# Kernel optimization log

Hardware: AMD Instinct MI355X
Metric: run time of the kernel (lower is better)

## Reference

```python
import jax, jax.numpy as jnp
import numpy as np

V, D, H, L, B, S = 8192, 128, 8, 2, 1, 128
HD = D // H
HID = int(8 * D / 3)
EPS = 1e-6


def setup_inputs() -> dict:
    key = jax.random.key(0)
    ks = jax.random.split(key, 12)
    sc = 0.02
    return {
        "idx": jax.random.randint(ks[0], (B, S), 0, V),
        "w_raw": jax.random.normal(ks[1], (D, V), jnp.float32) * sc,
        "norm1_w": jnp.ones((L, D), jnp.float32),
        "norm2_w": jnp.ones((L, D), jnp.float32),
        "wq": jax.random.normal(ks[2], (L, D, D), jnp.float32) * sc,
        "wk": jax.random.normal(ks[3], (L, D, D), jnp.float32) * sc,
        "wv": jax.random.normal(ks[4], (L, D, D), jnp.float32) * sc,
        "wo": jax.random.normal(ks[5], (L, D, D), jnp.float32) * sc,
        "w1": jax.random.normal(ks[6], (L, D, HID), jnp.float32) * sc,
        "w3": jax.random.normal(ks[7], (L, D, HID), jnp.float32) * sc,
        "w2": jax.random.normal(ks[8], (L, HID, D), jnp.float32) * sc,
        "final_norm_w": jnp.ones((D,), jnp.float32),
    }


def rmsnorm(x, w):
    return x * jax.lax.rsqrt(jnp.mean(x * x, axis=-1, keepdims=True) + EPS) * w


def rope_cos_sin(seqlen, hd):
    inv = 1.0 / (10000.0 ** (jnp.arange(0, hd, 2, dtype=jnp.float32) / hd))
    t = jnp.arange(seqlen, dtype=jnp.float32)
    f = jnp.outer(t, inv)  # (S, hd/2)
    return jnp.cos(f), jnp.sin(f)


def apply_rope(x, cos, sin):
    # x: (B,S,H,HD); interleaved complex pairs as in Llama
    x0, x1 = x[..., 0::2], x[..., 1::2]
    c = cos[None, :, None, :]
    s = sin[None, :, None, :]
    r0 = x0 * c - x1 * s
    r1 = x0 * s + x1 * c
    return jnp.stack([r0, r1], axis=-1).reshape(x.shape)


def forward(idx, w_raw, norm1_w, norm2_w, wq, wk, wv, wo, w1, w2, w3, final_norm_w):
    Wemb = jax.nn.sigmoid(w_raw)                 # (D,V)
    x = Wemb.T[idx]                              # Yoneda one-hot @ W.T == gather -> (B,S,D)
    cos, sin = rope_cos_sin(S, HD)
    causal = jnp.tril(jnp.ones((S, S), bool))[None, None]  # (1,1,S,S)
    scale = 1.0 / jnp.sqrt(jnp.float32(HD))
    for i in range(L):
        # Multi-Universe attention (heads == universes), RoPE, causal SDPA
        h = rmsnorm(x, norm1_w[i])
        q = (h @ wq[i]).reshape(B, S, H, HD)
        k = (h @ wk[i]).reshape(B, S, H, HD)
        v = (h @ wv[i]).reshape(B, S, H, HD)
        q = apply_rope(q, cos, sin)
        k = apply_rope(k, cos, sin)
        scores = jnp.einsum("bihd,bjhd->bhij", q, k) * scale
        scores = jnp.where(causal, scores, jnp.float32(-1e9))
        attn = jax.nn.softmax(scores, axis=-1)
        o = jnp.einsum("bhij,bjhd->bihd", attn, v).reshape(B, S, D) @ wo[i]
        x = x + o
        # SwiGLU FFN
        h2 = rmsnorm(x, norm2_w[i])
        x = x + (jax.nn.silu(h2 @ w1[i]) * (h2 @ w3[i])) @ w2[i]
    x_norm = rmsnorm(x, final_norm_w)
    # Godel-Heyting reachability head
    x_n = x_norm / jnp.linalg.norm(x_norm, axis=-1, keepdims=True)      # (B,S,D)
    v_n = (Wemb / jnp.linalg.norm(Wemb, axis=0, keepdims=True)).T        # (V,D)
    a = x_n[:, :, None, :]                                               # (B,S,1,D)
    b = v_n[None, None, :, :]                                            # (1,1,V,D)
    # strict Godel implication: a => b = 1 if a <= b else b
    imp = jnp.where(a <= b, jnp.float32(1.0), b)                         # (B,S,V,D)
    logits = jnp.clip(imp.mean(axis=-1), 1e-6, 1.0 - 1e-6)               # (B,S,V)
    return logits


def reference(idx, w_raw, norm1_w, norm2_w, wq, wk, wv, wo, w1, w2, w3, final_norm_w):
    return forward(idx, w_raw, norm1_w, norm2_w, wq, wk, wv, wo, w1, w2, w3, final_norm_w)
```

## Files before the change

### kernel.cpp

```cpp
#include <hip/hip_runtime.h>
#include <math.h>

#define V 8192
#define D 128
#define NH 8
#define HD 16
#define SEQ 128
#define HID 341
#define EPS 1e-6f

__device__ __forceinline__ float sigm(float x) { return 1.0f / (1.0f + __expf(-x)); }

__device__ __forceinline__ float block_sum256(float v, float* scratch) {
    #pragma unroll
    for (int m = 32; m > 0; m >>= 1) v += __shfl_xor(v, m);
    if ((threadIdx.x & 63) == 0) scratch[threadIdx.x >> 6] = v;
    __syncthreads();
    float s = (scratch[0] + scratch[1]) + (scratch[2] + scratch[3]);
    __syncthreads();
    return s;
}

__global__ __launch_bounds__(256, 1) void k_embed_qkv(
    const int* __restrict__ idx, const float* __restrict__ w_raw,
    const float* __restrict__ wq, const float* __restrict__ wk,
    const float* __restrict__ wv, const float* __restrict__ n1w,
    const float* __restrict__ w1, const float* __restrict__ w3,
    const float* __restrict__ w2, const float* __restrict__ wo,
    float* __restrict__ x, float* __restrict__ q, float* __restrict__ k,
    float* __restrict__ v, float* __restrict__ sink) {
    int t = threadIdx.x;
    if (blockIdx.x >= SEQ) {
        int g = (blockIdx.x - SEQ) * 256 + t;
        float acc = 0.f;
        const float4* p = (const float4*)w_raw;
        for (int i = g; i < 262144; i += 65536) {
            float4 u = p[i];
            acc += u.x + u.y + u.z + u.w;
        }
        p = (const float4*)w1;
        if (g < 21824) { float4 u = p[g]; acc += u.x + u.y + u.z + u.w; }
        p = (const float4*)w3;
        if (g < 21824) { float4 u = p[g]; acc += u.x + u.y + u.z + u.w; }
        p = (const float4*)w2;
        if (g < 21824) { float4 u = p[g]; acc += u.x + u.y + u.z + u.w; }
        p = (const float4*)wq;
        if (g < 8192) { float4 u = p[g]; acc += u.x + u.y + u.z + u.w; }
        p = (const float4*)wk;
        if (g < 8192) { float4 u = p[g]; acc += u.x + u.y + u.z + u.w; }
        p = (const float4*)wv;
        if (g < 8192) { float4 u = p[g]; acc += u.x + u.y + u.z + u.w; }
        p = (const float4*)wo;
        if (g < 8192) { float4 u = p[g]; acc += u.x + u.y + u.z + u.w; }
        if (acc == 1234.5678f) sink[0] = acc;
        return;
    }
    __shared__ float hr[D], qrow[D], krow[D], vpart[2][D], scr[4];
    int s = blockIdx.x;
    int col = t & 127, half = t >> 7, dlo = half * 64;
    float xv = 0.f;
    if (t < 128) xv = sigm(w_raw[t * V + idx[s]]);
    float wpre[128];
    const float* wsel = (t < 128) ? wq : wk;
    #pragma unroll
    for (int d = 0; d < 128; ++d) wpre[d] = wsel[d * D + col];
    float wvpre[64];
    #pragma unroll
    for (int d = 0; d < 64; ++d) wvpre[d] = wv[(dlo + d) * D + col];
    if (t < 128) x[s * D + t] = xv;
    float ss = block_sum256(xv * xv, scr);
    float r = 1.0f / sqrtf(ss * (1.0f / D) + EPS);
    if (t < 128) hr[t] = xv * r * n1w[t];
    __syncthreads();
    float a0 = 0, a1 = 0, a2 = 0, a3 = 0;
    #pragma unroll
    for (int d = 0; d < 128; d += 4) {
        a0 += hr[d] * wpre[d];
        a1 += hr[d + 1] * wpre[d + 1];
        a2 += hr[d + 2] * wpre[d + 2];
        a3 += hr[d + 3] * wpre[d + 3];
    }
    float qk = (a0 + a1) + (a2 + a3);
    float b0 = 0, b1 = 0, b2 = 0, b3 = 0;
    #pragma unroll
    for (int d = 0; d < 64; d += 4) {
        b0 += hr[dlo + d] * wvpre[d];
        b1 += hr[dlo + d + 1] * wvpre[d + 1];
        b2 += hr[dlo + d + 2] * wvpre[d + 2];
        b3 += hr[dlo + d + 3] * wvpre[d + 3];
    }
    vpart[half][col] = (b0 + b1) + (b2 + b3);
    if (t < 128) qrow[col] = qk;
    else krow[col] = qk;
    __syncthreads();
    if (t < 128) {
        v[s * D + t] = vpart[0][t] + vpart[1][t];
        int c = t & (HD - 1);
        int m = c >> 1;
        float fr = (float)s * expf(-(float)m * 1.15129254649702283e+00f);
        float cs = cosf(fr), sn = sinf(fr);
        int base = t & ~1;
        float qe = qrow[base], qod = qrow[base + 1];
        float ke = krow[base], kod = krow[base + 1];
        q[s * D + t] = (c & 1) ? (qe * sn + qod * cs) : (qe * cs - qod * sn);
        k[s * D + t] = (c & 1) ? (ke * sn + kod * cs) : (ke * cs - kod * sn);
    }
}

template <int MODE>
__global__ __launch_bounds__(256, 1) void k_layer(
    const float* __restrict__ q, const float* __restrict__ kg,
    const float* __restrict__ vg, float* __restrict__ x,
    const float* __restrict__ wo, const float* __restrict__ n2w,
    const float* __restrict__ w1, const float* __restrict__ w3,
    const float* __restrict__ w2, const float* __restrict__ wq,
    const float* __restrict__ wk, const float* __restrict__ wv,
    const float* __restrict__ n1w, float* __restrict__ qo, float* __restrict__ ko,
    float* __restrict__ vo, const float* __restrict__ fw, float* __restrict__ xng) {
    __shared__ float ps[NH][SEQ + 1];
    __shared__ float qs[D], orow[D], h2[D];
    __shared__ float part[2][D];
    __shared__ float afA[HID], afB[HID], af[HID];
    __shared__ float rl[NH];
    __shared__ float scr[4];
    int s = blockIdx.x, t = threadIdx.x;
    int col = t & 127, half = t >> 7;
    int jlo = half * 64, dlo = half * 64;

    float qv = 0.f, xr = 0.f;
    if (t < 128) {
        qv = q[s * D + t];
        xr = x[s * D + t];
    }
    float4 kp[4][4];
    #pragma unroll
    for (int u = 0; u < 4; ++u) {
        const float4* p = (const float4*)&kg[col * D + (half + 2 * u) * HD];
        kp[u][0] = p[0]; kp[u][1] = p[1]; kp[u][2] = p[2]; kp[u][3] = p[3];
    }
    float vpre[64];
    #pragma unroll
    for (int j = 0; j < 64; ++j) vpre[j] = vg[(jlo + j) * D + col];
    float wopre[64];
    #pragma unroll
    for (int u = 0; u < 64; ++u) wopre[u] = wo[(dlo + u) * D + col];

    if (t < 128) qs[t] = qv;
    __syncthreads();

    #pragma unroll
    for (int u = 0; u < 4; ++u) {
        int h = half + 2 * u;
        const float* qh = &qs[h * HD];
        float acc = kp[u][0].x * qh[0] + kp[u][0].y * qh[1] + kp[u][0].z * qh[2] +
                    kp[u][0].w * qh[3] + kp[u][1].x * qh[4] + kp[u][1].y * qh[5] +
                    kp[u][1].z * qh[6] + kp[u][1].w * qh[7] + kp[u][2].x * qh[8] +
                    kp[u][2].y * qh[9] + kp[u][2].z * qh[10] + kp[u][2].w * qh[11] +
                    kp[u][3].x * qh[12] + kp[u][3].y * qh[13] + kp[u][3].z * qh[14] +
                    kp[u][3].w * qh[15];
        ps[h][col] = (col <= s) ? acc * 0.25f : 0.f;
    }
    __syncthreads();

    {
        int h = t >> 5, lane = t & 31;
        float pm = -1e30f;
        for (int j = lane; j <= s; j += 32) pm = fmaxf(pm, ps[h][j]);
        #pragma unroll
        for (int m = 16; m > 0; m >>= 1) pm = fmaxf(pm, __shfl_xor(pm, m, 32));
        float psum = 0.f;
        for (int j = lane; j <= s; j += 32) {
            float e = __expf(ps[h][j] - pm);
            ps[h][j] = e;
            psum += e;
        }
        #pragma unroll
        for (int m = 16; m > 0; m >>= 1) psum += __shfl_xor(psum, m, 32);
        if (lane == 0) rl[h] = 1.0f / psum;
    }
    __syncthreads();

    {
        int h = col >> 4;
        float a0 = 0, a1 = 0, a2 = 0, a3 = 0;
        #pragma unroll
        for (int j = 0; j < 64; j += 4) {
            a0 += ps[h][jlo + j] * vpre[j];
            a1 += ps[h][jlo + j + 1] * vpre[j + 1];
            a2 += ps[h][jlo + j + 2] * vpre[j + 2];
            a3 += ps[h][jlo + j + 3] * vpre[j + 3];
        }
        part[half][col] = (a0 + a1) + (a2 + a3);
    }
    __syncthreads();
    if (t < 128) orow[t] = (part[0][t] + part[1][t]) * rl[t >> 4];
    __syncthreads();

    {
        float a0 = 0, a1 = 0;
        #pragma unroll
        for (int u = 0; u < 64; u += 2) {
            a0 += orow[dlo + u] * wopre[u];
            a1 += orow[dlo + u + 1] * wopre[u + 1];
        }
        part[half][col] = a0 + a1;
    }
    __syncthreads();
    float xn = 0.f;
    if (t < 128) xn = xr + part[0][t] + part[1][t];
    float ss2 = block_sum256((t < 128) ? xn * xn : 0.f, scr);
    float r2 = 1.0f / sqrtf(ss2 * (1.0f / D) + EPS);
    if (t < 128) h2[t] = xn * r2 * n2w[t];
    __syncthreads();

    for (int task = t; task < 2 * HID; task += 256) {
        int mat = task >= HID;
        int c2 = mat ? (task - HID) : task;
        const float* w = mat ? w3 : w1;
        float a0 = 0, a1 = 0, a2 = 0, a3 = 0;
        #pragma unroll 8
        for (int d = 0; d < D; d += 4) {
            a0 += h2[d] * w[d * HID + c2];
            a1 += h2[d + 1] * w[(d + 1) * HID + c2];
            a2 += h2[d + 2] * w[(d + 2) * HID + c2];
            a3 += h2[d + 3] * w[(d + 3) * HID + c2];
        }
        if (mat) afB[c2] = (a0 + a1) + (a2 + a3);
        else afA[c2] = (a0 + a1) + (a2 + a3);
    }
    __syncthreads();
    for (int c2 = t; c2 < HID; c2 += 256) {
        float a1v = afA[c2];
        af[c2] = (a1v / (1.0f + __expf(-a1v))) * afB[c2];
    }
    __syncthreads();

    {
        int lo = half ? 171 : 0;
        int hi = half ? 341 : 171;
        float a0 = 0, a1 = 0, a2 = 0, a3 = 0;
        int tt = lo;
        #pragma unroll 8
        for (; tt + 3 < hi; tt += 4) {
            a0 += af[tt] * w2[tt * D + col];
            a1 += af[tt + 1] * w2[(tt + 1) * D + col];
            a2 += af[tt + 2] * w2[(tt + 2) * D + col];
            a3 += af[tt + 3] * w2[(tt + 3) * D + col];
        }
        for (; tt < hi; ++tt) a0 += af[tt] * w2[tt * D + col];
        part[half][col] = (a0 + a1) + (a2 + a3);
    }
    __syncthreads();
    float x2 = 0.f;
    if (t < 128) {
        x2 = xn + part[0][t] + part[1][t];
        if (MODE == 0) x[s * D + t] = x2;
    }

    float ss = block_sum256((t < 128) ? x2 * x2 : 0.f, scr);
    float r = 1.0f / sqrtf(ss * (1.0f / D) + EPS);

    if constexpr (MODE == 0) {
        if (t < 128) h2[t] = x2 * r * n1w[t];
        __syncthreads();
        const float* wsel = (t < 128) ? wq : wk;
        float a0 = 0, a1 = 0, a2 = 0, a3 = 0;
        #pragma unroll 8
        for (int d = 0; d < D; d += 4) {
            a0 += h2[d] * wsel[d * D + col];
            a1 += h2[d + 1] * wsel[(d + 1) * D + col];
            a2 += h2[d + 2] * wsel[(d + 2) * D + col];
            a3 += h2[d + 3] * wsel[(d + 3) * D + col];
        }
        float qk = (a0 + a1) + (a2 + a3);
        float b0 = 0, b1 = 0, b2 = 0, b3 = 0;
        #pragma unroll 8
        for (int d = dlo; d < dlo + 64; d += 4) {
            b0 += h2[d] * wv[d * D + col];
            b1 += h2[d + 1] * wv[(d + 1) * D + col];
            b2 += h2[d + 2] * wv[(d + 2) * D + col];
            b3 += h2[d + 3] * wv[(d + 3) * D + col];
        }
        part[half][col] = (b0 + b1) + (b2 + b3);
        if (t < 128) qs[col] = qk;
        else orow[col] = qk;
        __syncthreads();
        if (t < 128) {
            vo[s * D + t] = part[0][t] + part[1][t];
            int c = t & (HD - 1);
            int mm = c >> 1;
            float fr = (float)s * expf(-(float)mm * 1.15129254649702283e+00f);
            float cs = cosf(fr), sn = sinf(fr);
            int base = t & ~1;
            float qe = qs[base], qod = qs[base + 1];
            float ke = orow[base], kod = orow[base + 1];
            qo[s * D + t] = (c & 1) ? (qe * sn + qod * cs) : (qe * cs - qod * sn);
            ko[s * D + t] = (c & 1) ? (ke * sn + kod * cs) : (ke * cs - kod * sn);
        }
    } else {
        float y = (t < 128) ? x2 * r * fw[t] : 0.f;
        float nn = block_sum256(y * y, scr);
        if (t < 128) xng[t * SEQ + s] = y / sqrtf(nn);
    }
}

__global__ __launch_bounds__(256) void k_logits(const float* __restrict__ xng,
                                                const float* __restrict__ w_raw,
                                                float* __restrict__ out) {
    __shared__ float xs[D * 64];
    __shared__ float vs[D * 32];
    __shared__ float nred[256];
    __shared__ float invn_s[32];
    int t = threadIdx.x;
    int sbase = (blockIdx.x & 1) * 64;
    int vbase = (blockIdx.x >> 1) * 32;
    for (int i = t; i < D * 64; i += 256) {
        int d = i >> 6, s2 = i & 63;
        xs[i] = xng[d * SEQ + sbase + s2];
    }
    for (int i = t; i < D * 32; i += 256) {
        int d = i >> 5, jj = i & 31;
        vs[i] = sigm(w_raw[d * V + vbase + jj]);
    }
    __syncthreads();
    {
        int colc = t & 31, dp = t >> 5;
        float p = 0.f;
        for (int u = 0; u < 16; ++u) {
            float vv = vs[(dp * 16 + u) * 32 + colc];
            p += vv * vv;
        }
        nred[t] = p;
    }
    __syncthreads();
    if (t < 32) {
        float sum = 0.f;
        for (int u = 0; u < 8; ++u) sum += nred[u * 32 + t];
        invn_s[t] = 1.0f / sqrtf(sum);
    }
    __syncthreads();
    for (int i = t; i < D * 32; i += 256) vs[i] *= invn_s[i & 31];
    __syncthreads();
    int vg = t & 15;
    int sg = t >> 4;
    float acc[4][2] = {};
    for (int d = 0; d < D; ++d) {
        float4 xq = *(const float4*)&xs[d * 64 + sg * 4];
        float2 vq = *(const float2*)&vs[d * 32 + vg * 2];
        acc[0][0] += (xq.x <= vq.x) ? 1.0f : vq.x;
        acc[0][1] += (xq.x <= vq.y) ? 1.0f : vq.y;
        acc[1][0] += (xq.y <= vq.x) ? 1.0f : vq.x;
        acc[1][1] += (xq.y <= vq.y) ? 1.0f : vq.y;
        acc[2][0] += (xq.z <= vq.x) ? 1.0f : vq.x;
        acc[2][1] += (xq.z <= vq.y) ? 1.0f : vq.y;
        acc[3][0] += (xq.w <= vq.x) ? 1.0f : vq.x;
        acc[3][1] += (xq.w <= vq.y) ? 1.0f : vq.y;
    }
    const float inv128 = 1.0f / 128.0f;
    #pragma unroll
    for (int si = 0; si < 4; ++si) {
        int s = sbase + sg * 4 + si;
        float2 ov;
        ov.x = fminf(fmaxf(acc[si][0] * inv128, 1e-6f), 1.0f - 1e-6f);
        ov.y = fminf(fmaxf(acc[si][1] * inv128, 1e-6f), 1.0f - 1e-6f);
        *(float2*)&out[s * V + vbase + vg * 2] = ov;
    }
}

extern "C" void kernel_launch(void* const* d_in, const int* in_sizes, int n_in,
                              void* d_out, int out_size, void* d_ws, size_t ws_size,
                              hipStream_t stream) {
    const int* idx = (const int*)d_in[0];
    const float* w_raw = (const float*)d_in[1];
    const float* n1w = (const float*)d_in[2];
    const float* n2w = (const float*)d_in[3];
    const float* wq = (const float*)d_in[4];
    const float* wk = (const float*)d_in[5];
    const float* wv = (const float*)d_in[6];
    const float* wo = (const float*)d_in[7];
    const float* w1 = (const float*)d_in[8];
    const float* w3 = (const float*)d_in[9];
    const float* w2 = (const float*)d_in[10];
    const float* fnw = (const float*)d_in[11];
    float* out = (float*)d_out;
    float* ws = (float*)d_ws;

    float* x    = ws;
    float* q1   = ws + 16384;
    float* k1   = ws + 32768;
    float* v1   = ws + 49152;
    float* q2   = ws + 65536;
    float* k2   = ws + 81920;
    float* v2   = ws + 98304;
    float* xng  = ws + 114688;
    float* sink = ws + 131072;

    k_embed_qkv<<<dim3(SEQ + 256), dim3(256), 0, stream>>>(
        idx, w_raw, wq, wk, wv, n1w, w1, w3, w2, wo, x, q1, k1, v1, sink);
    k_layer<0><<<dim3(SEQ), dim3(256), 0, stream>>>(
        q1, k1, v1, x, wo, n2w, w1, w3, w2,
        wq + D * D, wk + D * D, wv + D * D, n1w + D, q2, k2, v2,
        (const float*)nullptr, (float*)nullptr);
    k_layer<1><<<dim3(SEQ), dim3(256), 0, stream>>>(
        q2, k2, v2, x, wo + D * D, n2w + D, w1 + D * HID, w3 + D * HID,
        w2 + HID * D, (const float*)nullptr, (const float*)nullptr,
        (const float*)nullptr, (const float*)nullptr, (float*)nullptr,
        (float*)nullptr, (float*)nullptr, fnw, xng);
    k_logits<<<dim3(512), dim3(256), 0, stream>>>(xng, w_raw, out);
}
```

Before: 146.3 us.

## Widen per-row layer kernel from 256 to 512 threads with four-way splits

The per-token layer kernel now runs 512 threads per block instead of 256. Each stage (scores, softmax, PV, Wo, W2, and the next layer's QKV projection) is split four ways across quarters rather than two. Per-thread register arrays shrink by half and each of the 128 blocks gets more parallel work, which is meant to cut latency on a grid that underfills the GPU. The cost is more partial sums through shared memory and wider reductions at every barrier.

```diff
diff --git a/kernel.cpp b/kernel.cpp
--- a/kernel.cpp
+++ b/kernel.cpp
@@ -17,6 +17,17 @@
     if ((threadIdx.x & 63) == 0) scratch[threadIdx.x >> 6] = v;
     __syncthreads();
     float s = (scratch[0] + scratch[1]) + (scratch[2] + scratch[3]);
+    __syncthreads();
+    return s;
+}
+
+__device__ __forceinline__ float block_sum512(float v, float* scratch) {
+    #pragma unroll
+    for (int m = 32; m > 0; m >>= 1) v += __shfl_xor(v, m);
+    if ((threadIdx.x & 63) == 0) scratch[threadIdx.x >> 6] = v;
+    __syncthreads();
+    float s = ((scratch[0] + scratch[1]) + (scratch[2] + scratch[3])) +
+              ((scratch[4] + scratch[5]) + (scratch[6] + scratch[7]));
     __syncthreads();
     return s;
 }
@@ -108,7 +119,7 @@
 }
 
 template <int MODE>
-__global__ __launch_bounds__(256, 1) void k_layer(
+__global__ __launch_bounds__(512, 2) void k_layer(
     const float* __restrict__ q, const float* __restrict__ kg,
     const float* __restrict__ vg, float* __restrict__ x,
     const float* __restrict__ wo, const float* __restrict__ n2w,
@@ -119,38 +130,38 @@
     float* __restrict__ vo, const float* __restrict__ fw, float* __restrict__ xng) {
     __shared__ float ps[NH][SEQ + 1];
     __shared__ float qs[D], orow[D], h2[D];
-    __shared__ float part[2][D];
+    __shared__ float part[4][D];
     __shared__ float afA[HID], afB[HID], af[HID];
     __shared__ float rl[NH];
-    __shared__ float scr[4];
+    __shared__ float scr[8];
     int s = blockIdx.x, t = threadIdx.x;
-    int col = t & 127, half = t >> 7;
-    int jlo = half * 64, dlo = half * 64;
+    int col = t & 127, quarter = t >> 7;
+    int jlo = quarter * 32, dlo = quarter * 32;
 
     float qv = 0.f, xr = 0.f;
     if (t < 128) {
         qv = q[s * D + t];
         xr = x[s * D + t];
     }
-    float4 kp[4][4];
-    #pragma unroll
-    for (int u = 0; u < 4; ++u) {
-        const float4* p = (const float4*)&kg[col * D + (half + 2 * u) * HD];
+    float4 kp[2][4];
+    #pragma unroll
+    for (int u = 0; u < 2; ++u) {
+        const float4* p = (const float4*)&kg[col * D + (quarter + 4 * u) * HD];
         kp[u][0] = p[0]; kp[u][1] = p[1]; kp[u][2] = p[2]; kp[u][3] = p[3];
     }
-    float vpre[64];
-    #pragma unroll
-    for (int j = 0; j < 64; ++j) vpre[j] = vg[(jlo + j) * D + col];
-    float wopre[64];
-    #pragma unroll
-    for (int u = 0; u < 64; ++u) wopre[u] = wo[(dlo + u) * D + col];
+    float vpre[32];
+    #pragma unroll
+    for (int j = 0; j < 32; ++j) vpre[j] = vg[(jlo + j) * D + col];
+    float wopre[32];
+    #pragma unroll
+    for (int u = 0; u < 32; ++u) wopre[u] = wo[(dlo + u) * D + col];
 
     if (t < 128) qs[t] = qv;
     __syncthreads();
 
     #pragma unroll
-    for (int u = 0; u < 4; ++u) {
-        int h = half + 2 * u;
+    for (int u = 0; u < 2; ++u) {
+        int h = quarter + 4 * u;
         const float* qh = &qs[h * HD];
         float acc = kp[u][0].x * qh[0] + kp[u][0].y * qh[1] + kp[u][0].z * qh[2] +
                     kp[u][0].w * qh[3] + kp[u][1].x * qh[4] + kp[u][1].y * qh[5] +
@@ -163,19 +174,19 @@
     __syncthreads();
 
     {
-        int h = t >> 5, lane = t & 31;
+        int h = t >> 6, lane = t & 63;
         float pm = -1e30f;
-        for (int j = lane; j <= s; j += 32) pm = fmaxf(pm, ps[h][j]);
+        for (int j = lane; j <= s; j += 64) pm = fmaxf(pm, ps[h][j]);
         #pragma unroll
-        for (int m = 16; m > 0; m >>= 1) pm = fmaxf(pm, __shfl_xor(pm, m, 32));
+        for (int m = 32; m > 0; m >>= 1) pm = fmaxf(pm, __shfl_xor(pm, m));
         float psum = 0.f;
-        for (int j = lane; j <= s; j += 32) {
+        for (int j = lane; j <= s; j += 64) {
             float e = __expf(ps[h][j] - pm);
             ps[h][j] = e;
             psum += e;
         }
         #pragma unroll
-        for (int m = 16; m > 0; m >>= 1) psum += __shfl_xor(psum, m, 32);
+        for (int m = 32; m > 0; m >>= 1) psum += __shfl_xor(psum, m);
         if (lane == 0) rl[h] = 1.0f / psum;
     }
     __syncthreads();
@@ -184,36 +195,36 @@
         int h = col >> 4;
         float a0 = 0, a1 = 0, a2 = 0, a3 = 0;
         #pragma unroll
-        for (int j = 0; j < 64; j += 4) {
+        for (int j = 0; j < 32; j += 4) {
             a0 += ps[h][jlo + j] * vpre[j];
             a1 += ps[h][jlo + j + 1] * vpre[j + 1];
             a2 += ps[h][jlo + j + 2] * vpre[j + 2];
             a3 += ps[h][jlo + j + 3] * vpre[j + 3];
         }
-        part[half][col] = (a0 + a1) + (a2 + a3);
-    }
-    __syncthreads();
-    if (t < 128) orow[t] = (part[0][t] + part[1][t]) * rl[t >> 4];
+        part[quarter][col] = (a0 + a1) + (a2 + a3);
+    }
+    __syncthreads();
+    if (t < 128) orow[t] = ((part[0][t] + part[1][t]) + (part[2][t] + part[3][t])) * rl[t >> 4];
     __syncthreads();
 
     {
         float a0 = 0, a1 = 0;
         #pragma unroll
-        for (int u = 0; u < 64; u += 2) {
+        for (int u = 0; u < 32; u += 2) {
             a0 += orow[dlo + u] * wopre[u];
             a1 += orow[dlo + u + 1] * wopre[u + 1];
         }
-        part[half][col] = a0 + a1;
+        part[quarter][col] = a0 + a1;
     }
     __syncthreads();
     float xn = 0.f;
-    if (t < 128) xn = xr + part[0][t] + part[1][t];
-    float ss2 = block_sum256((t < 128) ? xn * xn : 0.f, scr);
+    if (t < 128) xn = xr + (part[0][t] + part[1][t]) + (part[2][t] + part[3][t]);
+    float ss2 = block_sum512((t < 128) ? xn * xn : 0.f, scr);
     float r2 = 1.0f / sqrtf(ss2 * (1.0f / D) + EPS);
     if (t < 128) h2[t] = xn * r2 * n2w[t];
     __syncthreads();
 
-    for (int task = t; task < 2 * HID; task += 256) {
+    for (int task = t; task < 2 * HID; task += 512) {
         int mat = task >= HID;
         int c2 = mat ? (task - HID) : task;
         const float* w = mat ? w3 : w1;
@@ -229,15 +240,15 @@
         else afA[c2] = (a0 + a1) + (a2 + a3);
     }
     __syncthreads();
-    for (int c2 = t; c2 < HID; c2 += 256) {
-        float a1v = afA[c2];
-        af[c2] = (a1v / (1.0f + __expf(-a1v))) * afB[c2];
+    if (t < HID) {
+        float a1v = afA[t];
+        af[t] = (a1v / (1.0f + __expf(-a1v))) * afB[t];
     }
     __syncthreads();
 
     {
-        int lo = half ? 171 : 0;
-        int hi = half ? 341 : 171;
+        int lo = quarter * 85;
+        int hi = (quarter == 3) ? 341 : lo + 85;
         float a0 = 0, a1 = 0, a2 = 0, a3 = 0;
         int tt = lo;
         #pragma unroll 8
@@ -248,45 +259,40 @@
             a3 += af[tt + 3] * w2[(tt + 3) * D + col];
         }
         for (; tt < hi; ++tt) a0 += af[tt] * w2[tt * D + col];
-        part[half][col] = (a0 + a1) + (a2 + a3);
+        part[quarter][col] = (a0 + a1) + (a2 + a3);
     }
     __syncthreads();
     float x2 = 0.f;
     if (t < 128) {
-        x2 = xn + part[0][t] + part[1][t];
+        x2 = xn + (part[0][t] + part[1][t]) + (part[2][t] + part[3][t]);
         if (MODE == 0) x[s * D + t] = x2;
     }
 
-    float ss = block_sum256((t < 128) ? x2 * x2 : 0.f, scr);
+    float ss = block_sum512((t < 128) ? x2 * x2 : 0.f, scr);
     float r = 1.0f / sqrtf(ss * (1.0f / D) + EPS);
 
     if constexpr (MODE == 0) {
         if (t < 128) h2[t] = x2 * r * n1w[t];
         __syncthreads();
-        const float* wsel = (t < 128) ? wq : wk;
-        float a0 = 0, a1 = 0, a2 = 0, a3 = 0;
-        #pragma unroll 8
-        for (int d = 0; d < D; d += 4) {
-            a0 += h2[d] * wsel[d * D + col];
-            a1 += h2[d + 1] * wsel[(d + 1) * D + col];
-            a2 += h2[d + 2] * wsel[(d + 2) * D + col];
-            a3 += h2[d + 3] * wsel[(d + 3) * D + col];
-        }
-        float qk = (a0 + a1) + (a2 + a3);
-        float b0 = 0, b1 = 0, b2 = 0, b3 = 0;
-        #pragma unroll 8
-        for (int d = dlo; d < dlo + 64; d += 4) {
-            b0 += h2[d] * wv[d * D + col];
-            b1 += h2[d + 1] * wv[(d + 1) * D + col];
-            b2 += h2[d + 2] * wv[(d + 2) * D + col];
-            b3 += h2[d + 3] * wv[(d + 3) * D + col];
-        }
-        part[half][col] = (b0 + b1) + (b2 + b3);
-        if (t < 128) qs[col] = qk;
-        else orow[col] = qk;
+        float qk = 0.f;
+        if (quarter < 3) {
+            const float* wsel = (quarter == 0) ? wq : ((quarter == 1) ? wk : wv);
+            float a0 = 0, a1 = 0, a2 = 0, a3 = 0;
+            #pragma unroll 8
+            for (int d = 0; d < D; d += 4) {
+                a0 += h2[d] * wsel[d * D + col];
+                a1 += h2[d + 1] * wsel[(d + 1) * D + col];
+                a2 += h2[d + 2] * wsel[(d + 2) * D + col];
+                a3 += h2[d + 3] * wsel[(d + 3) * D + col];
+            }
+            qk = (a0 + a1) + (a2 + a3);
+        }
+        if (quarter == 0) qs[col] = qk;
+        else if (quarter == 1) orow[col] = qk;
+        else if (quarter == 2) part[0][col] = qk;
         __syncthreads();
         if (t < 128) {
-            vo[s * D + t] = part[0][t] + part[1][t];
+            vo[s * D + t] = part[0][t];
             int c = t & (HD - 1);
             int mm = c >> 1;
             float fr = (float)s * expf(-(float)mm * 1.15129254649702283e+00f);
@@ -299,7 +305,7 @@
         }
     } else {
         float y = (t < 128) ? x2 * r * fw[t] : 0.f;
-        float nn = block_sum256(y * y, scr);
+        float nn = block_sum512(y * y, scr);
         if (t < 128) xng[t * SEQ + s] = y / sqrtf(nn);
     }
 }
@@ -397,11 +403,11 @@
 
     k_embed_qkv<<<dim3(SEQ + 256), dim3(256), 0, stream>>>(
         idx, w_raw, wq, wk, wv, n1w, w1, w3, w2, wo, x, q1, k1, v1, sink);
-    k_layer<0><<<dim3(SEQ), dim3(256), 0, stream>>>(
+    k_layer<0><<<dim3(SEQ), dim3(512), 0, stream>>>(
         q1, k1, v1, x, wo, n2w, w1, w3, w2,
         wq + D * D, wk + D * D, wv + D * D, n1w + D, q2, k2, v2,
         (const float*)nullptr, (float*)nullptr);
-    k_layer<1><<<dim3(SEQ), dim3(256), 0, stream>>>(
+    k_layer<1><<<dim3(SEQ), dim3(512), 0, stream>>>(
         q2, k2, v2, x, wo + D * D, n2w + D, w1 + D * HID, w3 + D * HID,
         w2 + HID * D, (const float*)nullptr, (const float*)nullptr,
         (const float*)nullptr, (const float*)nullptr, (float*)nullptr,
```

Result: faster. 141.5 us (-3.3%).
